# Performance work log

Measured on AMD Instinct MI355X. Metric: run time of the kernel, lower is better.

The kernel has to match this reference:

```python
import jax, jax.numpy as jnp
import numpy as np

B, T, D, F, E, K = 2, 1024, 1024, 2048, 8, 2

def setup_inputs() -> dict:
    key = jax.random.key(0)
    ks = jax.random.split(key, 9)
    s = 0.02
    return {
        "states": jax.random.normal(ks[0], (B, T, D), dtype=jnp.float32),
        "Wg": jax.random.normal(ks[1], (D, E), dtype=jnp.float32) * s,
        "W_in": jax.random.normal(ks[2], (E, D, F), dtype=jnp.float32) * s,
        "b_in": jnp.zeros((E, F), dtype=jnp.float32),
        "W_scale": jax.random.normal(ks[3], (E, D, F), dtype=jnp.float32) * s,
        "b_scale": jnp.zeros((E, F), dtype=jnp.float32),
        "W_out": jax.random.normal(ks[4], (E, F, D), dtype=jnp.float32) * s,
        "b_out": jnp.zeros((E, D), dtype=jnp.float32),
        "num_selected": K,
    }

def reference(states, Wg, W_in, b_in, W_scale, b_scale, W_out, b_out, num_selected):
    b, t, d = states.shape
    x = states.reshape(-1, d)                      # [N, D]
    n = x.shape[0]
    # router: softmax over experts, then top-k + renormalize
    probs = jax.nn.softmax(x @ Wg, axis=-1)        # [N, E]
    topw, topi = jax.lax.top_k(probs, num_selected)  # [N, K]
    topw = topw / topw.sum(axis=-1, keepdims=True)
    # dense combine weights [N, E]: zero except selected experts
    w_full = jnp.zeros_like(probs).at[jnp.arange(n)[:, None], topi].set(topw)
    # gated-GELU expert MLPs, batched over experts
    h = jnp.einsum('nd,edf->enf', x, W_in) + b_in[:, None, :]       # [E, N, F]
    s = jnp.einsum('nd,edf->enf', x, W_scale) + b_scale[:, None, :]
    inner = jax.nn.gelu(h, approximate=False) * s                    # exact GELU (torch default)
    y = jnp.einsum('enf,efd->end', inner, W_out) + b_out[:, None, :]  # [E, N, D]
    out = jnp.einsum('end,ne->nd', y, w_full)                         # weighted combine
    return out.reshape(b, t, d)
```

## Files before the change

kernel.cpp:

```cpp
#include <hip/hip_runtime.h>
#include <hip/hip_bf16.h>
#include <math.h>

#define N_TOK 2048
#define DIM   1024
#define FF    2048
#define NEXP  8
#define NSLOT (N_TOK * 2)

typedef __attribute__((ext_vector_type(8))) short short8;
typedef __attribute__((ext_vector_type(4))) float f32x4;
typedef _Float16 half_t;
typedef __attribute__((ext_vector_type(4))) _Float16 h16x4;

__device__ __forceinline__ unsigned short f2bf(float f) {
    unsigned int u = __float_as_uint(f);
    u += 0x7FFFu + ((u >> 16) & 1u);
    return (unsigned short)(u >> 16);
}

#define GLOAD_LDS16(g, l) \
    __builtin_amdgcn_global_load_lds((const __attribute__((address_space(1))) unsigned int*)(g), \
                                     (__attribute__((address_space(3))) unsigned int*)(l), 16, 0, 0)

__global__ __launch_bounds__(256) void k_router(const float* __restrict__ x,
        const float* __restrict__ Wg, int* __restrict__ hdr,
        int* __restrict__ tok_e, float* __restrict__ tok_w) {
    int wave = threadIdx.x >> 6, lane = threadIdx.x & 63;
    int t = blockIdx.x * 4 + wave;
    float acc[NEXP];
#pragma unroll
    for (int e = 0; e < NEXP; ++e) acc[e] = 0.f;
    const float* xr = x + (size_t)t * DIM;
    for (int d = lane; d < DIM; d += 64) {
        float xv = xr[d];
        const float* wr = Wg + d * NEXP;
#pragma unroll
        for (int e = 0; e < NEXP; ++e) acc[e] += xv * wr[e];
    }
#pragma unroll
    for (int off = 32; off > 0; off >>= 1) {
#pragma unroll
        for (int e = 0; e < NEXP; ++e) acc[e] += __shfl_down(acc[e], off);
    }
    if (lane == 0) {
        int e0 = 0;
#pragma unroll
        for (int e = 1; e < NEXP; ++e) if (acc[e] > acc[e0]) e0 = e;
        int e1 = -1;
#pragma unroll
        for (int e = 0; e < NEXP; ++e) {
            if (e == e0) continue;
            if (e1 < 0 || acc[e] > acc[e1]) e1 = e;
        }
        float w0 = 1.f / (1.f + expf(acc[e1] - acc[e0]));
        tok_e[2 * t] = e0; tok_e[2 * t + 1] = e1;
        tok_w[2 * t] = w0; tok_w[2 * t + 1] = 1.f - w0;
        atomicAdd(&hdr[e0], 1);
        atomicAdd(&hdr[e1], 1);
    }
}

__global__ void k_scan(int* hdr) {
    if (threadIdx.x == 0 && blockIdx.x == 0) {
        int s = 0;
        for (int e = 0; e < NEXP; ++e) {
            hdr[16 + e] = s;
            hdr[8 + e]  = s;
            s += hdr[e];
        }
        hdr[24] = s;
    }
}

__global__ __launch_bounds__(256) void k_assign(const float* __restrict__ x,
        int* __restrict__ hdr, const int* __restrict__ tok_e,
        int* __restrict__ tok_slot, unsigned short* __restrict__ xg) {
    __shared__ int sh[2];
    int t = blockIdx.x;
    if (threadIdx.x == 0) {
        int e0 = tok_e[2 * t], e1 = tok_e[2 * t + 1];
        int p0 = atomicAdd(&hdr[8 + e0], 1);
        int p1 = atomicAdd(&hdr[8 + e1], 1);
        tok_slot[2 * t] = p0; tok_slot[2 * t + 1] = p1;
        sh[0] = p0; sh[1] = p1;
    }
    __syncthreads();
    int s0 = sh[0], s1 = sh[1];
    const float4* xr = (const float4*)(x + (size_t)t * DIM);
    float4 v = xr[threadIdx.x];
    ushort4 b;
    b.x = f2bf(v.x); b.y = f2bf(v.y); b.z = f2bf(v.z); b.w = f2bf(v.w);
    ((ushort4*)(xg + (size_t)s0 * DIM))[threadIdx.x] = b;
    ((ushort4*)(xg + (size_t)s1 * DIM))[threadIdx.x] = b;
}

__global__ __launch_bounds__(256, 4) void k_expert_hs(
        const unsigned short* __restrict__ xg,
        const float* __restrict__ Win, const float* __restrict__ Wsc,
        const float* __restrict__ b_in, const float* __restrict__ b_sc,
        const int* __restrict__ hdr, unsigned short* __restrict__ inner) {
    int e = blockIdx.z;
    int cnt = hdr[e];
    int mtile = blockIdx.y;
    if (mtile * 128 >= cnt) return;
    int base = hdr[16 + e];
    int f0 = blockIdx.x * 64;

    __shared__ unsigned short As[128 * 32];
    __shared__ unsigned short Bh[4 * 64 * 8];
    __shared__ unsigned short Bs[4 * 64 * 8];

    int tid = threadIdx.x;
    int wave = tid >> 6, lane = tid & 63;
    int lr = lane & 15, lq = lane >> 4;
    int wm = (wave >> 1) * 64, wf = (wave & 1) * 32;

    f32x4 acch[4][2], accs[4][2];
#pragma unroll
    for (int mi = 0; mi < 4; ++mi)
#pragma unroll
        for (int fi = 0; fi < 2; ++fi) {
            acch[mi][fi] = (f32x4){0.f, 0.f, 0.f, 0.f};
            accs[mi][fi] = (f32x4){0.f, 0.f, 0.f, 0.f};
        }

    const unsigned short* Arow = xg + (size_t)(base + mtile * 128) * DIM;
    int arow = wave * 16 + (lane >> 2);
    int akk  = (lane & 3) * 8;

    int bf = tid & 63, bkq = tid >> 6;
    const float* ph_base = Win + (size_t)e * DIM * FF + f0 + bf;
    const float* ps_base = Wsc + (size_t)e * DIM * FF + f0 + bf;

    unsigned hv[4], sv[4];
    {
        const float* ph = ph_base + (size_t)(bkq * 8) * FF;
        const float* ps = ps_base + (size_t)(bkq * 8) * FF;
#pragma unroll
        for (int j = 0; j < 4; ++j) {
            hv[j] = (unsigned)f2bf(ph[(size_t)(2 * j) * FF]) |
                    ((unsigned)f2bf(ph[(size_t)(2 * j + 1) * FF]) << 16);
            sv[j] = (unsigned)f2bf(ps[(size_t)(2 * j) * FF]) |
                    ((unsigned)f2bf(ps[(size_t)(2 * j + 1) * FF]) << 16);
        }
    }

    for (int k0 = 0; k0 < DIM; k0 += 32) {
        __syncthreads();
        const unsigned short* gA = Arow + (size_t)arow * DIM + k0 + akk;
        GLOAD_LDS16(gA, &As[(wave * 16) * 32]);
        GLOAD_LDS16(gA + (size_t)64 * DIM, &As[(64 + wave * 16) * 32]);
        *(uint4*)&Bh[(bkq * 64 + bf) * 8] = make_uint4(hv[0], hv[1], hv[2], hv[3]);
        *(uint4*)&Bs[(bkq * 64 + bf) * 8] = make_uint4(sv[0], sv[1], sv[2], sv[3]);
        __syncthreads();

        unsigned hvN[4], svN[4];
        bool more = (k0 + 32 < DIM);
        if (more) {
            const float* ph = ph_base + (size_t)(k0 + 32 + bkq * 8) * FF;
            const float* ps = ps_base + (size_t)(k0 + 32 + bkq * 8) * FF;
#pragma unroll
            for (int j = 0; j < 4; ++j) {
                hvN[j] = (unsigned)f2bf(ph[(size_t)(2 * j) * FF]) |
                         ((unsigned)f2bf(ph[(size_t)(2 * j + 1) * FF]) << 16);
                svN[j] = (unsigned)f2bf(ps[(size_t)(2 * j) * FF]) |
                         ((unsigned)f2bf(ps[(size_t)(2 * j + 1) * FF]) << 16);
            }
        }

        short8 af[4], bhf[2], bsf[2];
#pragma unroll
        for (int mi = 0; mi < 4; ++mi)
            af[mi] = *(const short8*)&As[(wm + mi * 16 + lr) * 32 + lq * 8];
#pragma unroll
        for (int fi = 0; fi < 2; ++fi) {
            bhf[fi] = *(const short8*)&Bh[(lq * 64 + wf + fi * 16 + lr) * 8];
            bsf[fi] = *(const short8*)&Bs[(lq * 64 + wf + fi * 16 + lr) * 8];
        }
#pragma unroll
        for (int mi = 0; mi < 4; ++mi)
#pragma unroll
            for (int fi = 0; fi < 2; ++fi) {
                acch[mi][fi] = __builtin_amdgcn_mfma_f32_16x16x32_bf16(
                    af[mi], bhf[fi], acch[mi][fi], 0, 0, 0);
                accs[mi][fi] = __builtin_amdgcn_mfma_f32_16x16x32_bf16(
                    af[mi], bsf[fi], accs[mi][fi], 0, 0, 0);
            }
        if (more) {
#pragma unroll
            for (int j = 0; j < 4; ++j) { hv[j] = hvN[j]; sv[j] = svN[j]; }
        }
    }

#pragma unroll
    for (int fi = 0; fi < 2; ++fi) {
        int f = f0 + wf + fi * 16 + lr;
        float bi = b_in[e * FF + f];
        float bs2 = b_sc[e * FF + f];
#pragma unroll
        for (int mi = 0; mi < 4; ++mi) {
#pragma unroll
            for (int r = 0; r < 4; ++r) {
                int rl = wm + mi * 16 + lq * 4 + r;
                int grow = mtile * 128 + rl;
                if (grow < cnt) {
                    float h = acch[mi][fi][r] + bi;
                    float s = accs[mi][fi][r] + bs2;
                    float g = 0.5f * h * (1.f + erff(h * 0.70710678f));
                    inner[(size_t)(base + grow) * FF + f] = f2bf(g * s);
                }
            }
        }
    }
}

__global__ __launch_bounds__(256, 4) void k_expert_out(
        const unsigned short* __restrict__ inner,
        const float* __restrict__ Wout,
        const int* __restrict__ hdr, half_t* __restrict__ pbuf) {
    int e = blockIdx.z & 7;
    int ks = blockIdx.z >> 3;
    int cnt = hdr[e];
    int mtile = blockIdx.y;
    if (mtile * 128 >= cnt) return;
    int base = hdr[16 + e];
    int d0 = blockIdx.x * 128;

    __shared__ unsigned short As[128 * 32];
    __shared__ unsigned short Bt[4 * 128 * 8];

    int tid = threadIdx.x;
    int wave = tid >> 6, lane = tid & 63;
    int lr = lane & 15, lq = lane >> 4;
    int wm = (wave >> 1) * 64, wn = (wave & 1) * 64;

    f32x4 acc[4][4];
#pragma unroll
    for (int mi = 0; mi < 4; ++mi)
#pragma unroll
        for (int ni = 0; ni < 4; ++ni) acc[mi][ni] = (f32x4){0.f, 0.f, 0.f, 0.f};

    const unsigned short* Arow = inner + (size_t)(base + mtile * 128) * FF;
    int arow = wave * 16 + (lane >> 2);
    int akk  = (lane & 3) * 8;

    int bd = tid & 127, bq = tid >> 7;
    const float* Wb = Wout + (size_t)e * FF * DIM + d0 + bd;

    int kbeg = ks * (FF / 2), kend = kbeg + FF / 2;

    unsigned wv[8];
    {
        const float* pw = Wb + (size_t)(kbeg + bq * 16) * DIM;
#pragma unroll
        for (int j = 0; j < 8; ++j)
            wv[j] = (unsigned)f2bf(pw[(size_t)(2 * j) * DIM]) |
                    ((unsigned)f2bf(pw[(size_t)(2 * j + 1) * DIM]) << 16);
    }

    for (int k0 = kbeg; k0 < kend; k0 += 32) {
        __syncthreads();
        const unsigned short* gA = Arow + (size_t)arow * FF + k0 + akk;
        GLOAD_LDS16(gA, &As[(wave * 16) * 32]);
        GLOAD_LDS16(gA + (size_t)64 * FF, &As[(64 + wave * 16) * 32]);
        *(uint4*)&Bt[((2 * bq) * 128 + bd) * 8]     = make_uint4(wv[0], wv[1], wv[2], wv[3]);
        *(uint4*)&Bt[((2 * bq + 1) * 128 + bd) * 8] = make_uint4(wv[4], wv[5], wv[6], wv[7]);
        __syncthreads();

        unsigned wvN[8];
        bool more = (k0 + 32 < kend);
        if (more) {
            const float* pw = Wb + (size_t)(k0 + 32 + bq * 16) * DIM;
#pragma unroll
            for (int j = 0; j < 8; ++j)
                wvN[j] = (unsigned)f2bf(pw[(size_t)(2 * j) * DIM]) |
                         ((unsigned)f2bf(pw[(size_t)(2 * j + 1) * DIM]) << 16);
        }

        short8 af[4], bfm[4];
#pragma unroll
        for (int mi = 0; mi < 4; ++mi)
            af[mi] = *(const short8*)&As[(wm + mi * 16 + lr) * 32 + lq * 8];
#pragma unroll
        for (int ni = 0; ni < 4; ++ni)
            bfm[ni] = *(const short8*)&Bt[(lq * 128 + wn + ni * 16 + lr) * 8];
#pragma unroll
        for (int mi = 0; mi < 4; ++mi)
#pragma unroll
            for (int ni = 0; ni < 4; ++ni)
                acc[mi][ni] = __builtin_amdgcn_mfma_f32_16x16x32_bf16(
                    af[mi], bfm[ni], acc[mi][ni], 0, 0, 0);
        if (more) {
#pragma unroll
            for (int j = 0; j < 8; ++j) wv[j] = wvN[j];
        }
    }

    half_t* P = pbuf + (size_t)ks * NSLOT * DIM;
#pragma unroll
    for (int ni = 0; ni < 4; ++ni) {
        int d = d0 + wn + ni * 16 + lr;
#pragma unroll
        for (int mi = 0; mi < 4; ++mi) {
#pragma unroll
            for (int r = 0; r < 4; ++r) {
                int rl = wm + mi * 16 + lq * 4 + r;
                int grow = mtile * 128 + rl;
                if (grow < cnt)
                    P[(size_t)(base + grow) * DIM + d] = (half_t)acc[mi][ni][r];
            }
        }
    }
}

__global__ __launch_bounds__(256) void k_combine(const half_t* __restrict__ pbuf,
        const int* __restrict__ tok_slot, const int* __restrict__ tok_e,
        const float* __restrict__ tok_w, const float* __restrict__ b_out,
        float* __restrict__ out) {
    int t = blockIdx.x;
    int d = threadIdx.x * 4;
    int s0 = tok_slot[2 * t], s1 = tok_slot[2 * t + 1];
    int e0 = tok_e[2 * t], e1 = tok_e[2 * t + 1];
    float w0 = tok_w[2 * t], w1 = tok_w[2 * t + 1];
    const half_t* pA = pbuf;
    const half_t* pB = pbuf + (size_t)NSLOT * DIM;
    h16x4 a0 = *(const h16x4*)&pA[(size_t)s0 * DIM + d];
    h16x4 a1 = *(const h16x4*)&pB[(size_t)s0 * DIM + d];
    h16x4 c0 = *(const h16x4*)&pA[(size_t)s1 * DIM + d];
    h16x4 c1 = *(const h16x4*)&pB[(size_t)s1 * DIM + d];
    float4 b0 = *(const float4*)&b_out[e0 * DIM + d];
    float4 b1 = *(const float4*)&b_out[e1 * DIM + d];
    float4 r;
    r.x = w0 * ((float)a0.x + (float)a1.x + b0.x) + w1 * ((float)c0.x + (float)c1.x + b1.x);
    r.y = w0 * ((float)a0.y + (float)a1.y + b0.y) + w1 * ((float)c0.y + (float)c1.y + b1.y);
    r.z = w0 * ((float)a0.z + (float)a1.z + b0.z) + w1 * ((float)c0.z + (float)c1.z + b1.z);
    r.w = w0 * ((float)a0.w + (float)a1.w + b0.w) + w1 * ((float)c0.w + (float)c1.w + b1.w);
    *(float4*)&out[(size_t)t * DIM + d] = r;
}

extern "C" void kernel_launch(void* const* d_in, const int* in_sizes, int n_in,
                              void* d_out, int out_size, void* d_ws, size_t ws_size,
                              hipStream_t stream) {
    (void)in_sizes; (void)n_in; (void)out_size; (void)ws_size;
    const float* x    = (const float*)d_in[0];
    const float* Wg   = (const float*)d_in[1];
    const float* Win  = (const float*)d_in[2];
    const float* b_in = (const float*)d_in[3];
    const float* Wsc  = (const float*)d_in[4];
    const float* b_sc = (const float*)d_in[5];
    const float* Wout = (const float*)d_in[6];
    const float* b_out= (const float*)d_in[7];
    float* out = (float*)d_out;

    char* ws = (char*)d_ws;
    int*   hdr      = (int*)ws;
    int*   tok_e    = (int*)(ws + 256);
    float* tok_w    = (float*)(ws + 16640);
    int*   tok_slot = (int*)(ws + 33024);
    unsigned short* xg    = (unsigned short*)(ws + 65792);
    unsigned short* inner = (unsigned short*)(ws + 65792 + 8388608);
    half_t* pbuf = (half_t*)(ws + 65792 + 8388608 + 16777216);

    hipMemsetAsync(hdr, 0, 256, stream);
    k_router<<<dim3(N_TOK / 4), dim3(256), 0, stream>>>(x, Wg, hdr, tok_e, tok_w);
    k_scan<<<dim3(1), dim3(64), 0, stream>>>(hdr);
    k_assign<<<dim3(N_TOK), dim3(256), 0, stream>>>(x, hdr, tok_e, tok_slot, xg);
    k_expert_hs<<<dim3(FF / 64, 16, NEXP), dim3(256), 0, stream>>>(xg, Win, Wsc, b_in, b_sc, hdr, inner);
    k_expert_out<<<dim3(DIM / 128, 16, NEXP * 2), dim3(256), 0, stream>>>(inner, Wout, hdr, pbuf);
    k_combine<<<dim3(N_TOK), dim3(256), 0, stream>>>(pbuf, tok_slot, tok_e, tok_w, b_out, out);
}
```

Before: 465.0 us.

## Pre-convert expert weights to transposed bf16 and load via direct-to-LDS

Adds a conversion kernel that transposes and converts all three expert weight tensors from fp32 to bf16 in a K-contiguous layout, run on every call before routing. Both expert GEMMs then load weight tiles with global_load_lds in the same way as the activation tiles, replacing strided per-element fp32 loads with register conversion and manual prefetch. This trades an extra full pass over the weights (read fp32, write bf16) for cheaper, coalesced weight streaming inside the GEMMs. The register-level software prefetch of the weights is dropped.

```diff
diff --git a/kernel.cpp b/kernel.cpp
--- a/kernel.cpp
+++ b/kernel.cpp
@@ -95,9 +95,37 @@
     ((ushort4*)(xg + (size_t)s1 * DIM))[threadIdx.x] = b;
 }
 
+__global__ __launch_bounds__(256) void k_cvt(const float* __restrict__ src,
+        unsigned short* __restrict__ dst, int R, int C) {
+    __shared__ unsigned short sh[64][65];
+    const float* S = src + (size_t)blockIdx.z * R * C;
+    unsigned short* Dp = dst + (size_t)blockIdx.z * R * C;
+    int c0 = blockIdx.x * 64, r0 = blockIdx.y * 64;
+    int t = threadIdx.x;
+    int rr = t >> 2, c4 = (t & 3) * 4;
+    const float* p = S + (size_t)(r0 + rr) * C + c0 + c4;
+#pragma unroll
+    for (int j = 0; j < 4; ++j) {
+        float4 v = *(const float4*)(p + 16 * j);
+        sh[rr][c4 + 16 * j + 0] = f2bf(v.x);
+        sh[rr][c4 + 16 * j + 1] = f2bf(v.y);
+        sh[rr][c4 + 16 * j + 2] = f2bf(v.z);
+        sh[rr][c4 + 16 * j + 3] = f2bf(v.w);
+    }
+    __syncthreads();
+    int oc = t >> 2, orr = (t & 3) * 16;
+    unsigned short tmp[16];
+#pragma unroll
+    for (int j = 0; j < 16; ++j) tmp[j] = sh[orr + j][oc];
+    unsigned short* q = Dp + (size_t)(c0 + oc) * R + r0 + orr;
+    *(uint4*)q       = *(uint4*)&tmp[0];
+    *(uint4*)(q + 8) = *(uint4*)&tmp[8];
+}
+
 __global__ __launch_bounds__(256, 4) void k_expert_hs(
         const unsigned short* __restrict__ xg,
-        const float* __restrict__ Win, const float* __restrict__ Wsc,
+        const unsigned short* __restrict__ Wth,
+        const unsigned short* __restrict__ Wts,
         const float* __restrict__ b_in, const float* __restrict__ b_sc,
         const int* __restrict__ hdr, unsigned short* __restrict__ inner) {
     int e = blockIdx.z;
@@ -108,8 +136,8 @@
     int f0 = blockIdx.x * 64;
 
     __shared__ unsigned short As[128 * 32];
-    __shared__ unsigned short Bh[4 * 64 * 8];
-    __shared__ unsigned short Bs[4 * 64 * 8];
+    __shared__ unsigned short Bh[64 * 32];
+    __shared__ unsigned short Bs[64 * 32];
 
     int tid = threadIdx.x;
     int wave = tid >> 6, lane = tid & 63;
@@ -125,49 +153,18 @@
             accs[mi][fi] = (f32x4){0.f, 0.f, 0.f, 0.f};
         }
 
-    const unsigned short* Arow = xg + (size_t)(base + mtile * 128) * DIM;
-    int arow = wave * 16 + (lane >> 2);
-    int akk  = (lane & 3) * 8;
-
-    int bf = tid & 63, bkq = tid >> 6;
-    const float* ph_base = Win + (size_t)e * DIM * FF + f0 + bf;
-    const float* ps_base = Wsc + (size_t)e * DIM * FF + f0 + bf;
-
-    unsigned hv[4], sv[4];
-    {
-        const float* ph = ph_base + (size_t)(bkq * 8) * FF;
-        const float* ps = ps_base + (size_t)(bkq * 8) * FF;
-#pragma unroll
-        for (int j = 0; j < 4; ++j) {
-            hv[j] = (unsigned)f2bf(ph[(size_t)(2 * j) * FF]) |
-                    ((unsigned)f2bf(ph[(size_t)(2 * j + 1) * FF]) << 16);
-            sv[j] = (unsigned)f2bf(ps[(size_t)(2 * j) * FF]) |
-                    ((unsigned)f2bf(ps[(size_t)(2 * j + 1) * FF]) << 16);
-        }
-    }
+    int lrow = lane >> 2, lcol = (lane & 3) * 8;
+    const unsigned short* Ab = xg  + (size_t)(base + mtile * 128 + wave * 16 + lrow) * DIM + lcol;
+    const unsigned short* Hb = Wth + ((size_t)e * FF + f0 + wave * 16 + lrow) * DIM + lcol;
+    const unsigned short* Sb = Wts + ((size_t)e * FF + f0 + wave * 16 + lrow) * DIM + lcol;
 
     for (int k0 = 0; k0 < DIM; k0 += 32) {
         __syncthreads();
-        const unsigned short* gA = Arow + (size_t)arow * DIM + k0 + akk;
-        GLOAD_LDS16(gA, &As[(wave * 16) * 32]);
-        GLOAD_LDS16(gA + (size_t)64 * DIM, &As[(64 + wave * 16) * 32]);
-        *(uint4*)&Bh[(bkq * 64 + bf) * 8] = make_uint4(hv[0], hv[1], hv[2], hv[3]);
-        *(uint4*)&Bs[(bkq * 64 + bf) * 8] = make_uint4(sv[0], sv[1], sv[2], sv[3]);
+        GLOAD_LDS16(Ab + k0, &As[(wave * 16) * 32]);
+        GLOAD_LDS16(Ab + k0 + (size_t)64 * DIM, &As[(64 + wave * 16) * 32]);
+        GLOAD_LDS16(Hb + k0, &Bh[(wave * 16) * 32]);
+        GLOAD_LDS16(Sb + k0, &Bs[(wave * 16) * 32]);
         __syncthreads();
-
-        unsigned hvN[4], svN[4];
-        bool more = (k0 + 32 < DIM);
-        if (more) {
-            const float* ph = ph_base + (size_t)(k0 + 32 + bkq * 8) * FF;
-            const float* ps = ps_base + (size_t)(k0 + 32 + bkq * 8) * FF;
-#pragma unroll
-            for (int j = 0; j < 4; ++j) {
-                hvN[j] = (unsigned)f2bf(ph[(size_t)(2 * j) * FF]) |
-                         ((unsigned)f2bf(ph[(size_t)(2 * j + 1) * FF]) << 16);
-                svN[j] = (unsigned)f2bf(ps[(size_t)(2 * j) * FF]) |
-                         ((unsigned)f2bf(ps[(size_t)(2 * j + 1) * FF]) << 16);
-            }
-        }
 
         short8 af[4], bhf[2], bsf[2];
 #pragma unroll
@@ -175,8 +172,8 @@
             af[mi] = *(const short8*)&As[(wm + mi * 16 + lr) * 32 + lq * 8];
 #pragma unroll
         for (int fi = 0; fi < 2; ++fi) {
-            bhf[fi] = *(const short8*)&Bh[(lq * 64 + wf + fi * 16 + lr) * 8];
-            bsf[fi] = *(const short8*)&Bs[(lq * 64 + wf + fi * 16 + lr) * 8];
+            bhf[fi] = *(const short8*)&Bh[(wf + fi * 16 + lr) * 32 + lq * 8];
+            bsf[fi] = *(const short8*)&Bs[(wf + fi * 16 + lr) * 32 + lq * 8];
         }
 #pragma unroll
         for (int mi = 0; mi < 4; ++mi)
@@ -187,10 +184,6 @@
                 accs[mi][fi] = __builtin_amdgcn_mfma_f32_16x16x32_bf16(
                     af[mi], bsf[fi], accs[mi][fi], 0, 0, 0);
             }
-        if (more) {
-#pragma unroll
-            for (int j = 0; j < 4; ++j) { hv[j] = hvN[j]; sv[j] = svN[j]; }
-        }
     }
 
 #pragma unroll
@@ -217,7 +210,7 @@
 
 __global__ __launch_bounds__(256, 4) void k_expert_out(
         const unsigned short* __restrict__ inner,
-        const float* __restrict__ Wout,
+        const unsigned short* __restrict__ Wto,
         const int* __restrict__ hdr, half_t* __restrict__ pbuf) {
     int e = blockIdx.z & 7;
     int ks = blockIdx.z >> 3;
@@ -228,7 +221,7 @@
     int d0 = blockIdx.x * 128;
 
     __shared__ unsigned short As[128 * 32];
-    __shared__ unsigned short Bt[4 * 128 * 8];
+    __shared__ unsigned short Bt[128 * 32];
 
     int tid = threadIdx.x;
     int wave = tid >> 6, lane = tid & 63;
@@ -241,42 +234,19 @@
 #pragma unroll
         for (int ni = 0; ni < 4; ++ni) acc[mi][ni] = (f32x4){0.f, 0.f, 0.f, 0.f};
 
-    const unsigned short* Arow = inner + (size_t)(base + mtile * 128) * FF;
-    int arow = wave * 16 + (lane >> 2);
-    int akk  = (lane & 3) * 8;
-
-    int bd = tid & 127, bq = tid >> 7;
-    const float* Wb = Wout + (size_t)e * FF * DIM + d0 + bd;
+    int lrow = lane >> 2, lcol = (lane & 3) * 8;
+    const unsigned short* Ab = inner + (size_t)(base + mtile * 128 + wave * 16 + lrow) * FF + lcol;
+    const unsigned short* Bb = Wto + ((size_t)e * DIM + d0 + wave * 16 + lrow) * FF + lcol;
 
     int kbeg = ks * (FF / 2), kend = kbeg + FF / 2;
-
-    unsigned wv[8];
-    {
-        const float* pw = Wb + (size_t)(kbeg + bq * 16) * DIM;
-#pragma unroll
-        for (int j = 0; j < 8; ++j)
-            wv[j] = (unsigned)f2bf(pw[(size_t)(2 * j) * DIM]) |
-                    ((unsigned)f2bf(pw[(size_t)(2 * j + 1) * DIM]) << 16);
-    }
 
     for (int k0 = kbeg; k0 < kend; k0 += 32) {
         __syncthreads();
-        const unsigned short* gA = Arow + (size_t)arow * FF + k0 + akk;
-        GLOAD_LDS16(gA, &As[(wave * 16) * 32]);
-        GLOAD_LDS16(gA + (size_t)64 * FF, &As[(64 + wave * 16) * 32]);
-        *(uint4*)&Bt[((2 * bq) * 128 + bd) * 8]     = make_uint4(wv[0], wv[1], wv[2], wv[3]);
-        *(uint4*)&Bt[((2 * bq + 1) * 128 + bd) * 8] = make_uint4(wv[4], wv[5], wv[6], wv[7]);
+        GLOAD_LDS16(Ab + k0, &As[(wave * 16) * 32]);
+        GLOAD_LDS16(Ab + k0 + (size_t)64 * FF, &As[(64 + wave * 16) * 32]);
+        GLOAD_LDS16(Bb + k0, &Bt[(wave * 16) * 32]);
+        GLOAD_LDS16(Bb + k0 + (size_t)64 * FF, &Bt[(64 + wave * 16) * 32]);
         __syncthreads();
-
-        unsigned wvN[8];
-        bool more = (k0 + 32 < kend);
-        if (more) {
-            const float* pw = Wb + (size_t)(k0 + 32 + bq * 16) * DIM;
-#pragma unroll
-            for (int j = 0; j < 8; ++j)
-                wvN[j] = (unsigned)f2bf(pw[(size_t)(2 * j) * DIM]) |
-                         ((unsigned)f2bf(pw[(size_t)(2 * j + 1) * DIM]) << 16);
-        }
 
         short8 af[4], bfm[4];
 #pragma unroll
@@ -284,17 +254,13 @@
             af[mi] = *(const short8*)&As[(wm + mi * 16 + lr) * 32 + lq * 8];
 #pragma unroll
         for (int ni = 0; ni < 4; ++ni)
-            bfm[ni] = *(const short8*)&Bt[(lq * 128 + wn + ni * 16 + lr) * 8];
+            bfm[ni] = *(const short8*)&Bt[(wn + ni * 16 + lr) * 32 + lq * 8];
 #pragma unroll
         for (int mi = 0; mi < 4; ++mi)
 #pragma unroll
             for (int ni = 0; ni < 4; ++ni)
                 acc[mi][ni] = __builtin_amdgcn_mfma_f32_16x16x32_bf16(
                     af[mi], bfm[ni], acc[mi][ni], 0, 0, 0);
-        if (more) {
-#pragma unroll
-            for (int j = 0; j < 8; ++j) wv[j] = wvN[j];
-        }
     }
 
     half_t* P = pbuf + (size_t)ks * NSLOT * DIM;
@@ -361,12 +327,18 @@
     unsigned short* xg    = (unsigned short*)(ws + 65792);
     unsigned short* inner = (unsigned short*)(ws + 65792 + 8388608);
     half_t* pbuf = (half_t*)(ws + 65792 + 8388608 + 16777216);
+    unsigned short* wt_h = (unsigned short*)(ws + 65792 + 8388608 + 16777216 + 16777216);
+    unsigned short* wt_s = wt_h + (size_t)NEXP * FF * DIM;
+    unsigned short* wt_o = wt_s + (size_t)NEXP * FF * DIM;
 
     hipMemsetAsync(hdr, 0, 256, stream);
+    k_cvt<<<dim3(FF / 64, DIM / 64, NEXP), dim3(256), 0, stream>>>(Win,  wt_h, DIM, FF);
+    k_cvt<<<dim3(FF / 64, DIM / 64, NEXP), dim3(256), 0, stream>>>(Wsc,  wt_s, DIM, FF);
+    k_cvt<<<dim3(DIM / 64, FF / 64, NEXP), dim3(256), 0, stream>>>(Wout, wt_o, FF, DIM);
     k_router<<<dim3(N_TOK / 4), dim3(256), 0, stream>>>(x, Wg, hdr, tok_e, tok_w);
     k_scan<<<dim3(1), dim3(64), 0, stream>>>(hdr);
     k_assign<<<dim3(N_TOK), dim3(256), 0, stream>>>(x, hdr, tok_e, tok_slot, xg);
-    k_expert_hs<<<dim3(FF / 64, 16, NEXP), dim3(256), 0, stream>>>(xg, Win, Wsc, b_in, b_sc, hdr, inner);
-    k_expert_out<<<dim3(DIM / 128, 16, NEXP * 2), dim3(256), 0, stream>>>(inner, Wout, hdr, pbuf);
+    k_expert_hs<<<dim3(FF / 64, 16, NEXP), dim3(256), 0, stream>>>(xg, wt_h, wt_s, b_in, b_sc, hdr, inner);
+    k_expert_out<<<dim3(DIM / 128, 16, NEXP * 2), dim3(256), 0, stream>>>(inner, wt_o, hdr, pbuf);
     k_combine<<<dim3(N_TOK), dim3(256), 0, stream>>>(pbuf, tok_slot, tok_e, tok_w, b_out, out);
 }
```

New measurement: 450.0 us. 3.2% less time.
